# Kernel optimization log

Measured on AMD Instinct MI355X. Metric: run time of the kernel, lower is better.

## Reference

```python
import jax, jax.numpy as jnp
import numpy as np

H = 32
W = 32
HIDDEN = 64
NUM_CLASSES = 10
BATCH = 128


def setup_inputs() -> dict:
    key = jax.random.key(0)
    ks = jax.random.split(key, 5)
    D = 4 * HIDDEN * H * W  # number_of_output_dimensions()
    return {
        "x": jax.random.normal(ks[0], (BATCH, 1, H, W), jnp.float32),
        "w_in": jax.random.normal(ks[1], (HIDDEN, 1), jnp.float32) * 0.1,
        "b_in": jnp.zeros((HIDDEN,), jnp.float32),
        "w_state": jax.random.normal(ks[2], (HIDDEN, HIDDEN, 2), jnp.float32) * (1.0 / np.sqrt(2 * HIDDEN)),
        "b_state": jnp.zeros((HIDDEN,), jnp.float32),
        "w_fc": jax.random.normal(ks[3], (D, NUM_CLASSES), jnp.float32) * 0.01,
        "b_fc": jnp.zeros((NUM_CLASSES,), jnp.float32),
    }


def _skew(x):
    # x: [B,1,H,W] -> [B,1,H,W+H-1]; row r shifted right by r (diagonal skew)
    Ws = W + H - 1
    col = jnp.arange(Ws)[None, :] - jnp.arange(H)[:, None]  # [H,Ws]
    valid = ((col >= 0) & (col < W)).astype(x.dtype)
    colc = jnp.clip(col, 0, W - 1)
    rows = jnp.arange(H)[:, None]
    return x[:, :, rows, colc] * valid[None, None]


def _one_direction(x, w_in, b_in, w_state, b_state):
    # Diagonal-scan MDRNN over skewed columns.
    B = x.shape[0]
    xs = _skew(x)  # [B,1,H,Ws]
    # Input projection for all columns at once (1x1 conv equivalent)
    xin = jnp.einsum('oc,bchw->bohw', w_in, xs) + b_in[None, :, None, None]
    cols = jnp.moveaxis(xin, 3, 0)  # [Ws,B,HIDDEN,H]

    w_up, w_same = w_state[:, :, 0], w_state[:, :, 1]

    def step(h, xc):
        # conv1d(kernel=2, padding=1) over column, bottom padding removed:
        # out[r] = w_up @ h[r-1] + w_same @ h[r]
        h_up = jnp.pad(h, ((0, 0), (0, 0), (1, 0)))[:, :, :H]
        s = (jnp.einsum('oi,bir->bor', w_up, h_up)
             + jnp.einsum('oi,bir->bor', w_same, h)
             + b_state[None, :, None])
        hn = jnp.tanh(s + xc)
        return hn, hn

    h0 = jnp.zeros((B, HIDDEN, H), x.dtype)
    _, ys = jax.lax.scan(step, h0, cols)  # [Ws,B,HIDDEN,H]
    acts = jnp.moveaxis(ys, 0, 3)  # [B,HIDDEN,H,Ws]
    # Unskew: out[..., r, c] = acts[..., r, c + r]
    ccols = jnp.arange(W)[None, :] + jnp.arange(H)[:, None]  # [H,W]
    rows = jnp.arange(H)[:, None]
    return acts[:, :, rows, ccols]  # [B,HIDDEN,H,W]


def reference(x, w_in, b_in, w_state, b_state, w_fc, b_fc):
    B = x.shape[0]
    # Four scanning directions via flips on dims 2 and 3, concatenated on batch
    x2 = x[:, :, ::-1, :]
    x3 = x[:, :, :, ::-1]
    x4 = x[:, :, ::-1, ::-1]
    xm = jnp.concatenate([x, x2, x3, x4], axis=0)  # [4B,1,H,W]
    acts = _one_direction(xm, w_in, b_in, w_state, b_state)  # [4B,HIDDEN,H,W]
    # index_select interleaving: example b gets its 4 direction copies contiguously
    sel = (jnp.arange(B)[:, None] + B * jnp.arange(4)[None, :]).reshape(-1)
    a = acts[sel].reshape(B, -1)  # [B, 4*HIDDEN*H*W]
    logits = a @ w_fc + b_fc
    return jax.nn.log_softmax(logits, axis=-1)
```

## Files before the change

### kernel.cpp

```cpp
#include <hip/hip_runtime.h>
#include <hip/hip_bf16.h>

#define NHID 64
#define NT   63
#define NBD  512
#define HLDS_STR 72
#define XSTR 35

typedef __attribute__((ext_vector_type(8))) short bf16x8;
typedef __attribute__((ext_vector_type(4))) float f32x4;

__device__ __forceinline__ float tanh_fast(float x) {
    const float e = __expf(2.0f * x);
    const float r = __builtin_amdgcn_rcpf(e + 1.0f);
    return 1.0f - 2.0f * r;
}

__device__ __forceinline__ unsigned int cvt_pk_bf16(float lo, float hi) {
    unsigned int r;
    asm("v_cvt_pk_bf16_f32 %0, %1, %2" : "=v"(r) : "v"(lo), "v"(hi));
    return r;
}

__device__ __forceinline__ float bf2f(unsigned int u16) {
    return __uint_as_float(u16 << 16);
}

#define SKEW_R0(t)  ((t) > 31 ? (t) - 31 : 0)
#define SKEW_R1(t)  ((t) < 31 ? (t) : 31)
#define SKEW_OFF(t) ((t) < 32 ? ((t) * ((t) + 1)) >> 1 : 1024 - (((63 - (t)) * (64 - (t))) >> 1))

#define LGKM_BARRIER() do {                                   \
    asm volatile("s_waitcnt lgkmcnt(0)" ::: "memory");        \
    __builtin_amdgcn_s_barrier();                             \
    asm volatile("" ::: "memory");                            \
} while (0)

__global__ __launch_bounds__(256, 2) void k_rnn(
    const float* __restrict__ x,
    const float* __restrict__ w_in,
    const float* __restrict__ b_in,
    const float* __restrict__ w_state,
    const float* __restrict__ b_state,
    unsigned short* __restrict__ acts_c)
{
    __shared__ __align__(16) unsigned short h0buf[33 * HLDS_STR];
    __shared__ __align__(16) unsigned short h1buf[33 * HLDS_STR];
    __shared__ float xs[32 * XSTR];

    const int tid = threadIdx.x;
    const int bd  = blockIdx.x;
    const int d   = bd >> 7;
    const int b   = bd & 127;
    const int lane = tid & 63;
    const int wave = tid >> 6;
    const int wp = wave & 1;
    const int nt = wave >> 1;
    const int n  = lane & 15;
    const int g  = lane >> 4;

    const bool flr = (d & 1) != 0;
    const bool flc = (d & 2) != 0;
    const float* xb = x + (size_t)b * 1024;
    for (int idx = tid; idx < 1024; idx += 256) {
        const int r = idx >> 5, c = idx & 31;
        xs[r * XSTR + c] = xb[(flr ? 31 - r : r) * 32 + (flc ? 31 - c : c)];
    }

    for (int m2 = tid; m2 < (33 * HLDS_STR) / 2; m2 += 256) {
        ((unsigned int*)h0buf)[m2] = 0u;
        ((unsigned int*)h1buf)[m2] = 0u;
    }

    bf16x8 a_hi[2][4], a_lo[2][4];
    #pragma unroll
    for (int wl = 0; wl < 2; ++wl) {
        const int o = wp * 32 + wl * 16 + n;
        #pragma unroll
        for (int kt = 0; kt < 4; ++kt) {
            const int s  = kt >> 1;
            const int cb = (kt & 1) * 32 + g * 8;
            bf16x8 hi8, lo8;
            #pragma unroll
            for (int j = 0; j < 8; ++j) {
                const float w = w_state[((size_t)o * 64 + cb + j) * 2 + s];
                const unsigned int hp = cvt_pk_bf16(w, 0.0f);
                const float wh = bf2f(hp & 0xffffu);
                const unsigned int lp = cvt_pk_bf16(w - wh, 0.0f);
                hi8[j] = (short)(hp & 0xffffu);
                lo8[j] = (short)(lp & 0xffffu);
            }
            a_hi[wl][kt] = hi8;
            a_lo[wl][kt] = lo8;
        }
    }

    float biasr[2][4], winr[2][4];
    #pragma unroll
    for (int wl = 0; wl < 2; ++wl)
        #pragma unroll
        for (int j = 0; j < 4; ++j) {
            const int o = wp * 32 + wl * 16 + g * 4 + j;
            biasr[wl][j] = b_in[o] + b_state[o];
            winr[wl][j]  = w_in[o];
        }

    const int r_out = nt * 16 + n;
    const int rdoff = r_out * HLDS_STR + g * 8;
    const int wroff = (r_out + 1) * HLDS_STR;
    const int cb0 = wp * 32 + g * 4;
    const int r_f = tid >> 3;
    const int sc  = (tid & 7) * 8;
    const int fl_off = (r_f + 1) * HLDS_STR + sc;

    unsigned short* actp = acts_c + (size_t)bd * 65536 + (size_t)r_f * 1984 + sc;
    int cc  = -r_out;
    int ccf = -r_f;
    const float* xs_r = &xs[r_out * XSTR];

    __syncthreads();

#define STEP(RB, WB) do {                                                       \
    const bf16x8 b0 = *(const bf16x8*)&RB[rdoff];                               \
    const bf16x8 b1 = *(const bf16x8*)&RB[rdoff + 32];                          \
    const bf16x8 b2 = *(const bf16x8*)&RB[rdoff + HLDS_STR];                    \
    const bf16x8 b3 = *(const bf16x8*)&RB[rdoff + HLDS_STR + 32];               \
    f32x4 a0h = {0,0,0,0}, a0l = {0,0,0,0}, a1h = {0,0,0,0}, a1l = {0,0,0,0};   \
    a0h = __builtin_amdgcn_mfma_f32_16x16x32_bf16(a_hi[0][0], b0, a0h, 0,0,0);  \
    a1h = __builtin_amdgcn_mfma_f32_16x16x32_bf16(a_hi[1][0], b0, a1h, 0,0,0);  \
    a0l = __builtin_amdgcn_mfma_f32_16x16x32_bf16(a_lo[0][0], b0, a0l, 0,0,0);  \
    a1l = __builtin_amdgcn_mfma_f32_16x16x32_bf16(a_lo[1][0], b0, a1l, 0,0,0);  \
    a0h = __builtin_amdgcn_mfma_f32_16x16x32_bf16(a_hi[0][1], b1, a0h, 0,0,0);  \
    a1h = __builtin_amdgcn_mfma_f32_16x16x32_bf16(a_hi[1][1], b1, a1h, 0,0,0);  \
    a0l = __builtin_amdgcn_mfma_f32_16x16x32_bf16(a_lo[0][1], b1, a0l, 0,0,0);  \
    a1l = __builtin_amdgcn_mfma_f32_16x16x32_bf16(a_lo[1][1], b1, a1l, 0,0,0);  \
    a0h = __builtin_amdgcn_mfma_f32_16x16x32_bf16(a_hi[0][2], b2, a0h, 0,0,0);  \
    a1h = __builtin_amdgcn_mfma_f32_16x16x32_bf16(a_hi[1][2], b2, a1h, 0,0,0);  \
    a0l = __builtin_amdgcn_mfma_f32_16x16x32_bf16(a_lo[0][2], b2, a0l, 0,0,0);  \
    a1l = __builtin_amdgcn_mfma_f32_16x16x32_bf16(a_lo[1][2], b2, a1l, 0,0,0);  \
    a0h = __builtin_amdgcn_mfma_f32_16x16x32_bf16(a_hi[0][3], b3, a0h, 0,0,0);  \
    a1h = __builtin_amdgcn_mfma_f32_16x16x32_bf16(a_hi[1][3], b3, a1h, 0,0,0);  \
    a0l = __builtin_amdgcn_mfma_f32_16x16x32_bf16(a_lo[0][3], b3, a0l, 0,0,0);  \
    a1l = __builtin_amdgcn_mfma_f32_16x16x32_bf16(a_lo[1][3], b3, a1l, 0,0,0);  \
    const float xv = ((unsigned)cc < 32u) ? xs_r[cc & 31] : 0.0f;               \
    {                                                                           \
        const float h0 = tanh_fast(a0h[0] + a0l[0] + biasr[0][0] + winr[0][0] * xv); \
        const float h1 = tanh_fast(a0h[1] + a0l[1] + biasr[0][1] + winr[0][1] * xv); \
        const float h2 = tanh_fast(a0h[2] + a0l[2] + biasr[0][2] + winr[0][2] * xv); \
        const float h3 = tanh_fast(a0h[3] + a0l[3] + biasr[0][3] + winr[0][3] * xv); \
        uint2 pk; pk.x = cvt_pk_bf16(h0, h1); pk.y = cvt_pk_bf16(h2, h3);       \
        *(uint2*)&WB[wroff + cb0] = pk;                                         \
    }                                                                           \
    {                                                                           \
        const float h0 = tanh_fast(a1h[0] + a1l[0] + biasr[1][0] + winr[1][0] * xv); \
        const float h1 = tanh_fast(a1h[1] + a1l[1] + biasr[1][1] + winr[1][1] * xv); \
        const float h2 = tanh_fast(a1h[2] + a1l[2] + biasr[1][2] + winr[1][2] * xv); \
        const float h3 = tanh_fast(a1h[3] + a1l[3] + biasr[1][3] + winr[1][3] * xv); \
        uint2 pk; pk.x = cvt_pk_bf16(h0, h1); pk.y = cvt_pk_bf16(h2, h3);       \
        *(uint2*)&WB[wroff + cb0 + 16] = pk;                                    \
    }                                                                           \
    LGKM_BARRIER();                                                             \
    const uint4 av = *(const uint4*)&WB[fl_off];                                \
    if ((unsigned)ccf < 32u) *(uint4*)actp = av;                                \
    actp += 64; ++cc; ++ccf;                                                    \
} while (0)

    for (int sp = 0; sp < 31; ++sp) {
        STEP(h0buf, h1buf);
        STEP(h1buf, h0buf);
    }
    STEP(h0buf, h1buf);
#undef STEP
}

__global__ __launch_bounds__(256) void k_prep(
    const float* __restrict__ w_fc,
    unsigned short* __restrict__ wt_swz)
{
    const int t = blockIdx.y;
    const int tid = threadIdx.x;
    const int r0 = SKEW_R0(t), r1 = SKEW_R1(t);
    const int cnt = r1 - r0 + 1;
    const int span = cnt << 10;
    int f = blockIdx.x * 2048 + tid * 8;
    const int fdst = f;
    if (f >= 4 * span) return;
    int d = 0;
    while (f >= span) { f -= span; ++d; }
    const int ks   = f >> 9;
    const int lane = (f >> 3) & 63;
    const int g = lane >> 4, n = lane & 15;
    unsigned int pk[4];
    #pragma unroll
    for (int jj = 0; jj < 4; ++jj) {
        float v[2] = {0.0f, 0.0f};
        #pragma unroll
        for (int h = 0; h < 2; ++h) {
            const int j = jj * 2 + h;
            const int k = ks * 32 + g * 8 + j;
            const int r = r0 + (k >> 6);
            const int o = k & 63;
            const int c = t - r;
            if (n < 10)
                v[h] = w_fc[((((size_t)(d * 64 + o)) << 10) + (r << 5) + c) * 10 + n];
        }
        pk[jj] = cvt_pk_bf16(v[0], v[1]);
    }
    uint4 st; st.x = pk[0]; st.y = pk[1]; st.z = pk[2]; st.w = pk[3];
    *(uint4*)(wt_swz + (size_t)SKEW_OFF(t) * 4096 + fdst) = st;
}

__global__ __launch_bounds__(256, 4) void k_fc(
    const unsigned short* __restrict__ acts_c,
    const unsigned short* __restrict__ wt_swz,
    float* __restrict__ partial)
{
    const int tid = threadIdx.x;
    const int blk = blockIdx.x;
    const int t   = blk >> 3;
    const int d   = (blk >> 1) & 3;
    const int mh  = blk & 1;
    const int lane = tid & 63;
    const int wv  = tid >> 6;
    const int g   = lane >> 4;
    const int n   = lane & 15;

    const int r0 = SKEW_R0(t), r1 = SKEW_R1(t);
    const int cnt = r1 - r0 + 1;
    const int off = SKEW_OFF(t);

    const int tb = d * 128 + mh * 64 + wv * 16;
    const unsigned short* Ap = acts_c + (size_t)(tb + n) * 65536
                             + (size_t)r0 * 1984 + (size_t)t * 64 + g * 8;
    const unsigned short* Bp = wt_swz
        + ((size_t)off * 4 + (size_t)d * cnt) * 1024 + lane * 8;

    f32x4 acc = {0.f, 0.f, 0.f, 0.f};
    #pragma unroll 2
    for (int q = 0; q < cnt; ++q) {
        const bf16x8 a0  = *(const bf16x8*)(Ap);
        const bf16x8 bb0 = *(const bf16x8*)(Bp);
        const bf16x8 a1  = *(const bf16x8*)(Ap + 32);
        const bf16x8 bb1 = *(const bf16x8*)(Bp + 512);
        acc = __builtin_amdgcn_mfma_f32_16x16x32_bf16(a0, bb0, acc, 0, 0, 0);
        acc = __builtin_amdgcn_mfma_f32_16x16x32_bf16(a1, bb1, acc, 0, 0, 0);
        Ap += 1984;
        Bp += 1024;
    }
    const int batch = tb + g * 4;
    #pragma unroll
    for (int reg = 0; reg < 4; ++reg)
        partial[((size_t)t * 512 + batch + reg) * 16 + n] = acc[reg];
}

__global__ __launch_bounds__(256) void k_out(
    const float* __restrict__ partial,
    const float* __restrict__ b_fc,
    float* __restrict__ out)
{
    __shared__ float lred[252 * 10];
    __shared__ float lgs[10];
    __shared__ float lse;
    const int b = blockIdx.x;
    const int tid = threadIdx.x;
    if (tid < 252) {
        const int t = tid >> 2, d = tid & 3;
        const float* p = partial + ((size_t)t * 512 + d * 128 + b) * 16;
        #pragma unroll
        for (int n2 = 0; n2 < 10; ++n2) lred[tid * 10 + n2] = p[n2];
    }
    __syncthreads();
    if (tid < 10) {
        float s = b_fc[tid];
        for (int i = 0; i < 252; ++i) s += lred[i * 10 + tid];
        lgs[tid] = s;
    }
    __syncthreads();
    if (tid == 0) {
        float m = lgs[0];
        for (int nn = 1; nn < 10; ++nn) m = fmaxf(m, lgs[nn]);
        float ssum = 0.0f;
        for (int nn = 0; nn < 10; ++nn) ssum += __expf(lgs[nn] - m);
        lse = m + __logf(ssum);
    }
    __syncthreads();
    if (tid < 10) out[b * 10 + tid] = lgs[tid] - lse;
}

extern "C" void kernel_launch(void* const* d_in, const int* in_sizes, int n_in,
                              void* d_out, int out_size, void* d_ws, size_t ws_size,
                              hipStream_t stream)
{
    const float* x       = (const float*)d_in[0];
    const float* w_in    = (const float*)d_in[1];
    const float* b_in    = (const float*)d_in[2];
    const float* w_state = (const float*)d_in[3];
    const float* b_state = (const float*)d_in[4];
    const float* w_fc    = (const float*)d_in[5];
    const float* b_fc    = (const float*)d_in[6];
    float* out = (float*)d_out;

    unsigned short* wt_swz = (unsigned short*)d_ws;
    float* partial = (float*)((char*)d_ws + (size_t)(8u << 20));
    unsigned short* acts_c = (unsigned short*)((char*)d_ws + (size_t)(16u << 20));

    k_prep<<<dim3(64, 63), 256, 0, stream>>>(w_fc, wt_swz);
    k_rnn <<<512, 256, 0, stream>>>(x, w_in, b_in, w_state, b_state, acts_c);
    k_fc  <<<504, 256, 0, stream>>>(acts_c, wt_swz, partial);
    k_out <<<128, 256, 0, stream>>>(partial, b_fc, out);
}
```

Baseline: 75.88 us.

## Split RNN recurrence over 8 waves per block and skip inactive diagonal row tiles

The recurrent kernel now launches 512 threads (8 waves) per block instead of 4. Each wave owns one 16-output by 16-row tile, so the MFMA and tanh chain per wave per step is half as long. Waves whose 16-row tile is not yet active (or already done) on the skewed diagonal skip the MFMA work for that step. Only the first 256 threads write activations out. In exchange, the block barrier each step now syncs twice as many waves, and the 512-thread launch bound may tighten per-thread register limits.

```diff
diff --git a/kernel.cpp b/kernel.cpp
--- a/kernel.cpp
+++ b/kernel.cpp
@@ -36,7 +36,7 @@
     asm volatile("" ::: "memory");                            \
 } while (0)
 
-__global__ __launch_bounds__(256, 2) void k_rnn(
+__global__ __launch_bounds__(512, 4) void k_rnn(
     const float* __restrict__ x,
     const float* __restrict__ w_in,
     const float* __restrict__ b_in,
@@ -54,28 +54,27 @@
     const int b   = bd & 127;
     const int lane = tid & 63;
     const int wave = tid >> 6;
-    const int wp = wave & 1;
-    const int nt = wave >> 1;
+    const int wo = wave >> 1;
+    const int wr = wave & 1;
     const int n  = lane & 15;
     const int g  = lane >> 4;
 
     const bool flr = (d & 1) != 0;
     const bool flc = (d & 2) != 0;
     const float* xb = x + (size_t)b * 1024;
-    for (int idx = tid; idx < 1024; idx += 256) {
+    for (int idx = tid; idx < 1024; idx += 512) {
         const int r = idx >> 5, c = idx & 31;
         xs[r * XSTR + c] = xb[(flr ? 31 - r : r) * 32 + (flc ? 31 - c : c)];
     }
 
-    for (int m2 = tid; m2 < (33 * HLDS_STR) / 2; m2 += 256) {
+    for (int m2 = tid; m2 < (33 * HLDS_STR) / 2; m2 += 512) {
         ((unsigned int*)h0buf)[m2] = 0u;
         ((unsigned int*)h1buf)[m2] = 0u;
     }
 
-    bf16x8 a_hi[2][4], a_lo[2][4];
-    #pragma unroll
-    for (int wl = 0; wl < 2; ++wl) {
-        const int o = wp * 32 + wl * 16 + n;
+    bf16x8 a_hi[4], a_lo[4];
+    {
+        const int o_a = wo * 16 + n;
         #pragma unroll
         for (int kt = 0; kt < 4; ++kt) {
             const int s  = kt >> 1;
@@ -83,93 +82,79 @@
             bf16x8 hi8, lo8;
             #pragma unroll
             for (int j = 0; j < 8; ++j) {
-                const float w = w_state[((size_t)o * 64 + cb + j) * 2 + s];
+                const float w = w_state[((size_t)o_a * 64 + cb + j) * 2 + s];
                 const unsigned int hp = cvt_pk_bf16(w, 0.0f);
                 const float wh = bf2f(hp & 0xffffu);
                 const unsigned int lp = cvt_pk_bf16(w - wh, 0.0f);
                 hi8[j] = (short)(hp & 0xffffu);
                 lo8[j] = (short)(lp & 0xffffu);
             }
-            a_hi[wl][kt] = hi8;
-            a_lo[wl][kt] = lo8;
+            a_hi[kt] = hi8;
+            a_lo[kt] = lo8;
         }
     }
 
-    float biasr[2][4], winr[2][4];
+    float biasr[4], winr[4];
     #pragma unroll
-    for (int wl = 0; wl < 2; ++wl)
-        #pragma unroll
-        for (int j = 0; j < 4; ++j) {
-            const int o = wp * 32 + wl * 16 + g * 4 + j;
-            biasr[wl][j] = b_in[o] + b_state[o];
-            winr[wl][j]  = w_in[o];
-        }
-
-    const int r_out = nt * 16 + n;
+    for (int j = 0; j < 4; ++j) {
+        const int o = wo * 16 + g * 4 + j;
+        biasr[j] = b_in[o] + b_state[o];
+        winr[j]  = w_in[o];
+    }
+
+    const int r_out = wr * 16 + n;
     const int rdoff = r_out * HLDS_STR + g * 8;
     const int wroff = (r_out + 1) * HLDS_STR;
-    const int cb0 = wp * 32 + g * 4;
+    const int cb0 = wo * 16 + g * 4;
+    const int tlo = wr * 16;
+    const float* xs_r = &xs[r_out * XSTR];
+
+    const bool flusher = tid < 256;
     const int r_f = tid >> 3;
     const int sc  = (tid & 7) * 8;
     const int fl_off = (r_f + 1) * HLDS_STR + sc;
-
     unsigned short* actp = acts_c + (size_t)bd * 65536 + (size_t)r_f * 1984 + sc;
-    int cc  = -r_out;
-    int ccf = -r_f;
-    const float* xs_r = &xs[r_out * XSTR];
-
-    __syncthreads();
-
-#define STEP(RB, WB) do {                                                       \
-    const bf16x8 b0 = *(const bf16x8*)&RB[rdoff];                               \
-    const bf16x8 b1 = *(const bf16x8*)&RB[rdoff + 32];                          \
-    const bf16x8 b2 = *(const bf16x8*)&RB[rdoff + HLDS_STR];                    \
-    const bf16x8 b3 = *(const bf16x8*)&RB[rdoff + HLDS_STR + 32];               \
-    f32x4 a0h = {0,0,0,0}, a0l = {0,0,0,0}, a1h = {0,0,0,0}, a1l = {0,0,0,0};   \
-    a0h = __builtin_amdgcn_mfma_f32_16x16x32_bf16(a_hi[0][0], b0, a0h, 0,0,0);  \
-    a1h = __builtin_amdgcn_mfma_f32_16x16x32_bf16(a_hi[1][0], b0, a1h, 0,0,0);  \
-    a0l = __builtin_amdgcn_mfma_f32_16x16x32_bf16(a_lo[0][0], b0, a0l, 0,0,0);  \
-    a1l = __builtin_amdgcn_mfma_f32_16x16x32_bf16(a_lo[1][0], b0, a1l, 0,0,0);  \
-    a0h = __builtin_amdgcn_mfma_f32_16x16x32_bf16(a_hi[0][1], b1, a0h, 0,0,0);  \
-    a1h = __builtin_amdgcn_mfma_f32_16x16x32_bf16(a_hi[1][1], b1, a1h, 0,0,0);  \
-    a0l = __builtin_amdgcn_mfma_f32_16x16x32_bf16(a_lo[0][1], b1, a0l, 0,0,0);  \
-    a1l = __builtin_amdgcn_mfma_f32_16x16x32_bf16(a_lo[1][1], b1, a1l, 0,0,0);  \
-    a0h = __builtin_amdgcn_mfma_f32_16x16x32_bf16(a_hi[0][2], b2, a0h, 0,0,0);  \
-    a1h = __builtin_amdgcn_mfma_f32_16x16x32_bf16(a_hi[1][2], b2, a1h, 0,0,0);  \
-    a0l = __builtin_amdgcn_mfma_f32_16x16x32_bf16(a_lo[0][2], b2, a0l, 0,0,0);  \
-    a1l = __builtin_amdgcn_mfma_f32_16x16x32_bf16(a_lo[1][2], b2, a1l, 0,0,0);  \
-    a0h = __builtin_amdgcn_mfma_f32_16x16x32_bf16(a_hi[0][3], b3, a0h, 0,0,0);  \
-    a1h = __builtin_amdgcn_mfma_f32_16x16x32_bf16(a_hi[1][3], b3, a1h, 0,0,0);  \
-    a0l = __builtin_amdgcn_mfma_f32_16x16x32_bf16(a_lo[0][3], b3, a0l, 0,0,0);  \
-    a1l = __builtin_amdgcn_mfma_f32_16x16x32_bf16(a_lo[1][3], b3, a1l, 0,0,0);  \
-    const float xv = ((unsigned)cc < 32u) ? xs_r[cc & 31] : 0.0f;               \
-    {                                                                           \
-        const float h0 = tanh_fast(a0h[0] + a0l[0] + biasr[0][0] + winr[0][0] * xv); \
-        const float h1 = tanh_fast(a0h[1] + a0l[1] + biasr[0][1] + winr[0][1] * xv); \
-        const float h2 = tanh_fast(a0h[2] + a0l[2] + biasr[0][2] + winr[0][2] * xv); \
-        const float h3 = tanh_fast(a0h[3] + a0l[3] + biasr[0][3] + winr[0][3] * xv); \
+
+    __syncthreads();
+
+#define STEP(T, RB, WB) do {                                                    \
+    if ((unsigned)((T) - tlo) < 48u) {                                          \
+        const bf16x8 b0 = *(const bf16x8*)&RB[rdoff];                           \
+        const bf16x8 b1 = *(const bf16x8*)&RB[rdoff + 32];                      \
+        const bf16x8 b2 = *(const bf16x8*)&RB[rdoff + HLDS_STR];                \
+        const bf16x8 b3 = *(const bf16x8*)&RB[rdoff + HLDS_STR + 32];           \
+        f32x4 ah = {0,0,0,0}, al = {0,0,0,0};                                   \
+        ah = __builtin_amdgcn_mfma_f32_16x16x32_bf16(a_hi[0], b0, ah, 0,0,0);   \
+        al = __builtin_amdgcn_mfma_f32_16x16x32_bf16(a_lo[0], b0, al, 0,0,0);   \
+        ah = __builtin_amdgcn_mfma_f32_16x16x32_bf16(a_hi[1], b1, ah, 0,0,0);   \
+        al = __builtin_amdgcn_mfma_f32_16x16x32_bf16(a_lo[1], b1, al, 0,0,0);   \
+        ah = __builtin_amdgcn_mfma_f32_16x16x32_bf16(a_hi[2], b2, ah, 0,0,0);   \
+        al = __builtin_amdgcn_mfma_f32_16x16x32_bf16(a_lo[2], b2, al, 0,0,0);   \
+        ah = __builtin_amdgcn_mfma_f32_16x16x32_bf16(a_hi[3], b3, ah, 0,0,0);   \
+        al = __builtin_amdgcn_mfma_f32_16x16x32_bf16(a_lo[3], b3, al, 0,0,0);   \
+        const int c_ = (T) - r_out;                                             \
+        const float xv = ((unsigned)c_ < 32u) ? xs_r[c_ & 31] : 0.0f;           \
+        const float h0 = tanh_fast(ah[0] + al[0] + biasr[0] + winr[0] * xv);    \
+        const float h1 = tanh_fast(ah[1] + al[1] + biasr[1] + winr[1] * xv);    \
+        const float h2 = tanh_fast(ah[2] + al[2] + biasr[2] + winr[2] * xv);    \
+        const float h3 = tanh_fast(ah[3] + al[3] + biasr[3] + winr[3] * xv);    \
         uint2 pk; pk.x = cvt_pk_bf16(h0, h1); pk.y = cvt_pk_bf16(h2, h3);       \
         *(uint2*)&WB[wroff + cb0] = pk;                                         \
     }                                                                           \
-    {                                                                           \
-        const float h0 = tanh_fast(a1h[0] + a1l[0] + biasr[1][0] + winr[1][0] * xv); \
-        const float h1 = tanh_fast(a1h[1] + a1l[1] + biasr[1][1] + winr[1][1] * xv); \
-        const float h2 = tanh_fast(a1h[2] + a1l[2] + biasr[1][2] + winr[1][2] * xv); \
-        const float h3 = tanh_fast(a1h[3] + a1l[3] + biasr[1][3] + winr[1][3] * xv); \
-        uint2 pk; pk.x = cvt_pk_bf16(h0, h1); pk.y = cvt_pk_bf16(h2, h3);       \
-        *(uint2*)&WB[wroff + cb0 + 16] = pk;                                    \
+    LGKM_BARRIER();                                                             \
+    if (flusher) {                                                              \
+        const uint4 av = *(const uint4*)&WB[fl_off];                            \
+        if ((unsigned)((T) - r_f) < 32u) *(uint4*)actp = av;                    \
+        actp += 64;                                                             \
     }                                                                           \
-    LGKM_BARRIER();                                                             \
-    const uint4 av = *(const uint4*)&WB[fl_off];                                \
-    if ((unsigned)ccf < 32u) *(uint4*)actp = av;                                \
-    actp += 64; ++cc; ++ccf;                                                    \
 } while (0)
 
     for (int sp = 0; sp < 31; ++sp) {
-        STEP(h0buf, h1buf);
-        STEP(h1buf, h0buf);
-    }
-    STEP(h0buf, h1buf);
+        const int t = 2 * sp;
+        STEP(t,     h0buf, h1buf);
+        STEP(t + 1, h1buf, h0buf);
+    }
+    STEP(62, h0buf, h1buf);
 #undef STEP
 }
 
@@ -305,7 +290,7 @@
     unsigned short* acts_c = (unsigned short*)((char*)d_ws + (size_t)(16u << 20));
 
     k_prep<<<dim3(64, 63), 256, 0, stream>>>(w_fc, wt_swz);
-    k_rnn <<<512, 256, 0, stream>>>(x, w_in, b_in, w_state, b_state, acts_c);
+    k_rnn <<<512, 512, 0, stream>>>(x, w_in, b_in, w_state, b_state, acts_c);
     k_fc  <<<504, 256, 0, stream>>>(acts_c, wt_swz, partial);
     k_out <<<128, 256, 0, stream>>>(partial, b_fc, out);
 }
```

After: 74.28 us. 1.02x faster.
